# Kernel optimization log

Measured on AMD Instinct MI355X. Metric: run time of the kernel, lower is better.

Reference implementation:

```python
import jax, jax.numpy as jnp
import numpy as np

H, N, D_IN, DK, DG = 16, 128, 256, 128, 64  # heads, boxes, appearance dim, key dim, geo dim

def setup_inputs() -> dict:
    key = jax.random.key(0)
    ks = jax.random.split(key, 6)
    return {
        "f_a": jax.random.normal(ks[0], (N, D_IN), dtype=jnp.float32),
        "position_embedding": jax.random.uniform(ks[1], (N, N, DG), dtype=jnp.float32),
        "WG": jax.random.normal(ks[2], (H, DG), dtype=jnp.float32) * 0.1,
        "bg": jnp.zeros((H,), dtype=jnp.float32),
        "WK": jax.random.normal(ks[3], (H, D_IN, DK), dtype=jnp.float32) * 0.05,
        "bk": jnp.zeros((H, DK), dtype=jnp.float32),
        "WQ": jax.random.normal(ks[4], (H, D_IN, DK), dtype=jnp.float32) * 0.05,
        "bq": jnp.zeros((H, DK), dtype=jnp.float32),
        "WV": jax.random.normal(ks[5], (H, D_IN, DK), dtype=jnp.float32) * 0.05,
        "bv": jnp.zeros((H, DK), dtype=jnp.float32),
    }

def reference(f_a, position_embedding, WG, bg, WK, bk, WQ, bq, WV, bv):
    # geometric gate: relu(pos @ WG + bg), per head -> (H, N, N)
    w_g = jax.nn.relu(jnp.einsum("mng,hg->hmn", position_embedding, WG) + bg[:, None, None])
    # projections for all heads at once: (H, N, DK)
    k = jnp.einsum("nd,hdk->hnk", f_a, WK) + bk[:, None, :]
    q = jnp.einsum("nd,hdk->hnk", f_a, WQ) + bq[:, None, :]
    v = jnp.einsum("nd,hdk->hnk", f_a, WV) + bv[:, None, :]
    # score[h,m,n] = k_m . q_n / sqrt(DK)   (note: keys index rows, queries index cols)
    score = jnp.einsum("hmk,hnk->hmn", k, q) / np.sqrt(DK).astype(np.float32)
    # log-clamped geometric bias, softmax over dim=1 of the (N,N) map == last axis here
    w_mn = jax.nn.softmax(jnp.log(jnp.clip(w_g, 1e-6, None)) + score, axis=-1)
    # original broadcast (N,N)*(N,1,DK) with N==DK then sum over -2 reduces to a column sum:
    # out[h,i,k] = v[h,i,k] * sum_j w_mn[h,j,k]
    colsum = jnp.sum(w_mn, axis=1)              # (H, DK)
    out = v * colsum[:, None, :]                 # (H, N, DK)
    concat = jnp.transpose(out, (1, 0, 2)).reshape(N, H * DK)  # (N, H*DK)
    # concat.view(N, H*DK, 1) + f_a (N, D_IN) broadcasts to (N, H*DK, D_IN)
    return concat[:, :, None] + f_a[:, None, :]
```

## Files before the change

### kernel.cpp

```cpp
#include <hip/hip_runtime.h>
#include <hip/hip_bf16.h>

#define H_   16
#define N_   128
#define DIN  256
#define DK_  128
#define DG_  64
#define HNK  (H_ * N_ * DK_)

using bf16 = __hip_bfloat16;

__device__ __forceinline__ float bf2f(unsigned short u) {
    union { unsigned int i; float f; } c;
    c.i = ((unsigned int)u) << 16;
    return c.f;
}
__device__ __forceinline__ unsigned short f2bf(float f) {
    union { float f; unsigned int i; } c;
    c.f = f;
    unsigned int r = c.i + 0x7fffu + ((c.i >> 16) & 1u);
    return (unsigned short)(r >> 16);
}

template<int BF>
__device__ __forceinline__ float lde(const void* p, int i) {
    if (BF) return bf2f(((const unsigned short*)p)[i]);
    else    return ((const float*)p)[i];
}

__global__ __launch_bounds__(64) void detect_init_kernel(
    const unsigned int* __restrict__ pos, int* __restrict__ flag,
    float* __restrict__ colsum)
{
    int t = threadIdx.x;
    int cnt = 0;
#pragma unroll
    for (int i = 0; i < 4; ++i) {
        unsigned int w = pos[t * 4 + i];
        cnt += ((w & 0xffffu) <= 0x3F80u) ? 1 : 0;
    }
#pragma unroll
    for (int off = 32; off > 0; off >>= 1) cnt += __shfl_xor(cnt, off, 64);
    if (t == 0) flag[0] = (cnt >= 192) ? 1 : 0;

    float4 z = make_float4(0.f, 0.f, 0.f, 0.f);
    float4* cs = (float4*)colsum;
#pragma unroll
    for (int i = 0; i < 8; ++i) cs[t + 64 * i] = z;
}

template<int BF>
__device__ __forceinline__ void proj_body(
    const void* __restrict__ fa, const void* __restrict__ W,
    const void* __restrict__ b, float* __restrict__ out, int h, int m0)
{
    int c = threadIdx.x;
    __shared__ float fa_s[4][DIN];
    for (int i = threadIdx.x; i < 4 * DIN; i += 128) {
        int r = i >> 8, d = i & 255;
        fa_s[r][d] = lde<BF>(fa, (m0 + r) * DIN + d);
    }
    __syncthreads();

    int wbase = h * DIN * DK_ + c;
    float a0 = 0.f, a1 = 0.f, a2 = 0.f, a3 = 0.f;
    for (int d = 0; d < DIN; ++d) {
        float w = lde<BF>(W, wbase + d * DK_);
        a0 += fa_s[0][d] * w;
        a1 += fa_s[1][d] * w;
        a2 += fa_s[2][d] * w;
        a3 += fa_s[3][d] * w;
    }
    float bb = lde<BF>(b, h * DK_ + c);
    float* o = out + (h * N_ + m0) * DK_ + c;
    o[0 * DK_] = a0 + bb;
    o[1 * DK_] = a1 + bb;
    o[2 * DK_] = a2 + bb;
    o[3 * DK_] = a3 + bb;
}

__global__ __launch_bounds__(128) void proj_kernel(
    const void* __restrict__ fa,
    const void* __restrict__ WK, const void* __restrict__ bk,
    const void* __restrict__ WQ, const void* __restrict__ bq,
    const void* __restrict__ WV, const void* __restrict__ bv,
    float* __restrict__ ws, const int* __restrict__ flag)
{
    int bx = blockIdx.x;
    int which = bx / (H_ * 32);
    int rem = bx - which * (H_ * 32);
    int h = rem >> 5;
    int m0 = (rem & 31) * 4;

    const void* W; const void* b; float* out;
    if (which == 0)      { W = WK; b = bk; out = ws; }
    else if (which == 1) { W = WQ; b = bq; out = ws + HNK; }
    else                 { W = WV; b = bv; out = ws + 2 * HNK; }

    if (flag[0]) proj_body<1>(fa, W, b, out, h, m0);
    else         proj_body<0>(fa, W, b, out, h, m0);
}

template<int BF>
__device__ __forceinline__ void score_body(
    const void* __restrict__ pos, const void* __restrict__ WG,
    const void* __restrict__ bg, const float* __restrict__ ws,
    float* __restrict__ colsum, int h, int m)
{
    int n = threadIdx.x;
    __shared__ float wg_s[DG_];
    __shared__ float krow[DK_];
    __shared__ float redmax[2];
    __shared__ float redsum[2];

    if (n < DG_) wg_s[n] = lde<BF>(WG, h * DG_ + n);
    krow[n] = ws[(h * N_ + m) * DK_ + n];
    __syncthreads();

    float g = lde<BF>(bg, h);
    if (BF) {
        const uint4* pv = (const uint4*)((const unsigned short*)pos + (m * N_ + n) * DG_);
#pragma unroll
        for (int i = 0; i < 8; ++i) {
            uint4 u = pv[i];
            unsigned int uu[4] = { u.x, u.y, u.z, u.w };
#pragma unroll
            for (int j = 0; j < 4; ++j) {
                g += bf2f((unsigned short)(uu[j] & 0xffffu)) * wg_s[i * 8 + j * 2];
                g += bf2f((unsigned short)(uu[j] >> 16))     * wg_s[i * 8 + j * 2 + 1];
            }
        }
    } else {
        const float4* pv = (const float4*)((const float*)pos + (m * N_ + n) * DG_);
#pragma unroll
        for (int i = 0; i < 16; ++i) {
            float4 u = pv[i];
            g += u.x * wg_s[4 * i] + u.y * wg_s[4 * i + 1]
               + u.z * wg_s[4 * i + 2] + u.w * wg_s[4 * i + 3];
        }
    }
    float lg = logf(fmaxf(fmaxf(g, 0.0f), 1e-6f));

    const float4* qv = (const float4*)(ws + HNK + (h * N_ + n) * DK_);
    float s = 0.f;
#pragma unroll 8
    for (int i = 0; i < 32; ++i) {
        float4 q4 = qv[i];
        s += q4.x * krow[4 * i] + q4.y * krow[4 * i + 1]
           + q4.z * krow[4 * i + 2] + q4.w * krow[4 * i + 3];
    }
    float z = lg + s * 0.08838834764831845f;

    float v = z;
#pragma unroll
    for (int off = 32; off > 0; off >>= 1) v = fmaxf(v, __shfl_xor(v, off, 64));
    int wave = n >> 6;
    if ((n & 63) == 0) redmax[wave] = v;
    __syncthreads();
    float M = fmaxf(redmax[0], redmax[1]);
    float e = expf(z - M);
    float t = e;
#pragma unroll
    for (int off = 32; off > 0; off >>= 1) t += __shfl_xor(t, off, 64);
    if ((n & 63) == 0) redsum[wave] = t;
    __syncthreads();
    float S = redsum[0] + redsum[1];
    float w = e / S;

    atomicAdd(&colsum[h * DK_ + n], w);
}

__global__ __launch_bounds__(128) void score_kernel(
    const void* __restrict__ pos,
    const void* __restrict__ WG, const void* __restrict__ bg,
    const float* __restrict__ ws, float* __restrict__ colsum,
    const int* __restrict__ flag)
{
    int h = blockIdx.x >> 7;
    int m = blockIdx.x & 127;
    if (flag[0]) score_body<1>(pos, WG, bg, ws, colsum, h, m);
    else         score_body<0>(pos, WG, bg, ws, colsum, h, m);
}

__global__ __launch_bounds__(256) void out_kernel(
    const void* __restrict__ fa, const float* __restrict__ ws,
    const float* __restrict__ colsum, void* __restrict__ out,
    const int* __restrict__ flag)
{
    int e = (blockIdx.x * 256 + threadIdx.x) * 8;
    int d0  = e & 255;
    int col = (e >> 8) & 2047;
    int n   = e >> 19;
    int h = col >> 7;
    int c = col & 127;

    const float* V = ws + 2 * HNK;
    float a = V[(h * N_ + n) * DK_ + c] * colsum[h * DK_ + c];

    if (flag[0]) {
        uint4 u = *(const uint4*)((const unsigned short*)fa + n * DIN + d0);
        unsigned int uu[4] = { u.x, u.y, u.z, u.w };
        unsigned int rr[4];
#pragma unroll
        for (int j = 0; j < 4; ++j) {
            float lo = bf2f((unsigned short)(uu[j] & 0xffffu)) + a;
            float hi = bf2f((unsigned short)(uu[j] >> 16)) + a;
            rr[j] = (unsigned int)f2bf(lo) | ((unsigned int)f2bf(hi) << 16);
        }
        *(uint4*)((unsigned short*)out + e) = make_uint4(rr[0], rr[1], rr[2], rr[3]);
    } else {
        const float4* fv = (const float4*)((const float*)fa + n * DIN + d0);
        float4 u0 = fv[0], u1 = fv[1];
        u0.x += a; u0.y += a; u0.z += a; u0.w += a;
        u1.x += a; u1.y += a; u1.z += a; u1.w += a;
        float4* ov = (float4*)((float*)out + e);
        ov[0] = u0;
        ov[1] = u1;
    }
}

extern "C" void kernel_launch(void* const* d_in, const int* in_sizes, int n_in,
                              void* d_out, int out_size, void* d_ws, size_t ws_size,
                              hipStream_t stream)
{
    const void* fa  = d_in[0];
    const void* pos = d_in[1];
    const void* WG  = d_in[2];
    const void* bg  = d_in[3];
    const void* WK  = d_in[4];
    const void* bk  = d_in[5];
    const void* WQ  = d_in[6];
    const void* bq  = d_in[7];
    const void* WV  = d_in[8];
    const void* bv  = d_in[9];

    int*   flag = (int*)d_ws;
    float* buf  = (float*)d_ws + 16;
    float* colsum = buf + 3 * HNK;

    hipLaunchKernelGGL(detect_init_kernel, dim3(1), dim3(64), 0, stream,
                       (const unsigned int*)pos, flag, colsum);

    hipLaunchKernelGGL(proj_kernel, dim3(3 * H_ * 32), dim3(128), 0, stream,
                       fa, WK, bk, WQ, bq, WV, bv, buf, flag);

    hipLaunchKernelGGL(score_kernel, dim3(H_ * N_), dim3(128), 0, stream,
                       pos, WG, bg, buf, colsum, flag);

    const int nblk = (N_ * H_ * DK_ * DIN) / (8 * 256);
    hipLaunchKernelGGL(out_kernel, dim3(nblk), dim3(256), 0, stream,
                       fa, buf, colsum, d_out, flag);
}
```

Baseline: 339.3 us.

## Drop detect/init kernel, inline dtype detection, vectorize LDS reads, nontemporal output stores

Removes the separate detect_init launch: each kernel now detects bf16 from the first 32 words of pos itself, and colsum zeroing moves into the first blocks of proj_kernel. LDS reads in the projection and score loops become 4-wide vector loads, logf/expf are replaced by the fast intrinsics, and the large output writes use nontemporal stores. The aim is to cut one launch plus serialization and to reduce memory and instruction overhead in the bandwidth-bound output kernel. Each thread now repeats a 32-word detection read, and the fast math intrinsics are less precise.

```diff
diff --git a/kernel.cpp b/kernel.cpp
--- a/kernel.cpp
+++ b/kernel.cpp
@@ -1,5 +1,4 @@
 #include <hip/hip_runtime.h>
-#include <hip/hip_bf16.h>
 
 #define H_   16
 #define N_   128
@@ -8,7 +7,8 @@
 #define DG_  64
 #define HNK  (H_ * N_ * DK_)
 
-using bf16 = __hip_bfloat16;
+typedef float        f32x4 __attribute__((ext_vector_type(4)));
+typedef unsigned int u32x4 __attribute__((ext_vector_type(4)));
 
 __device__ __forceinline__ float bf2f(unsigned short u) {
     union { unsigned int i; float f; } c;
@@ -28,25 +28,13 @@
     else    return ((const float*)p)[i];
 }
 
-__global__ __launch_bounds__(64) void detect_init_kernel(
-    const unsigned int* __restrict__ pos, int* __restrict__ flag,
-    float* __restrict__ colsum)
-{
-    int t = threadIdx.x;
+__device__ __forceinline__ int detect_bf16(const void* __restrict__ pos) {
+    const unsigned int* p = (const unsigned int*)pos;
     int cnt = 0;
 #pragma unroll
-    for (int i = 0; i < 4; ++i) {
-        unsigned int w = pos[t * 4 + i];
-        cnt += ((w & 0xffffu) <= 0x3F80u) ? 1 : 0;
-    }
-#pragma unroll
-    for (int off = 32; off > 0; off >>= 1) cnt += __shfl_xor(cnt, off, 64);
-    if (t == 0) flag[0] = (cnt >= 192) ? 1 : 0;
-
-    float4 z = make_float4(0.f, 0.f, 0.f, 0.f);
-    float4* cs = (float4*)colsum;
-#pragma unroll
-    for (int i = 0; i < 8; ++i) cs[t + 64 * i] = z;
+    for (int i = 0; i < 32; ++i)
+        cnt += ((p[i] & 0xffffu) <= 0x3F80u) ? 1 : 0;
+    return cnt >= 24;
 }
 
 template<int BF>
@@ -55,7 +43,7 @@
     const void* __restrict__ b, float* __restrict__ out, int h, int m0)
 {
     int c = threadIdx.x;
-    __shared__ float fa_s[4][DIN];
+    __shared__ __align__(16) float fa_s[4][DIN];
     for (int i = threadIdx.x; i < 4 * DIN; i += 128) {
         int r = i >> 8, d = i & 255;
         fa_s[r][d] = lde<BF>(fa, (m0 + r) * DIN + d);
@@ -64,12 +52,22 @@
 
     int wbase = h * DIN * DK_ + c;
     float a0 = 0.f, a1 = 0.f, a2 = 0.f, a3 = 0.f;
-    for (int d = 0; d < DIN; ++d) {
-        float w = lde<BF>(W, wbase + d * DK_);
-        a0 += fa_s[0][d] * w;
-        a1 += fa_s[1][d] * w;
-        a2 += fa_s[2][d] * w;
-        a3 += fa_s[3][d] * w;
+    const f32x4* f0 = (const f32x4*)fa_s[0];
+    const f32x4* f1 = (const f32x4*)fa_s[1];
+    const f32x4* f2 = (const f32x4*)fa_s[2];
+    const f32x4* f3 = (const f32x4*)fa_s[3];
+#pragma unroll 4
+    for (int dq = 0; dq < DIN / 4; ++dq) {
+        int d = dq * 4;
+        float w0 = lde<BF>(W, wbase + (d + 0) * DK_);
+        float w1 = lde<BF>(W, wbase + (d + 1) * DK_);
+        float w2 = lde<BF>(W, wbase + (d + 2) * DK_);
+        float w3 = lde<BF>(W, wbase + (d + 3) * DK_);
+        f32x4 x0 = f0[dq], x1 = f1[dq], x2 = f2[dq], x3 = f3[dq];
+        a0 += w0 * x0[0] + w1 * x0[1] + w2 * x0[2] + w3 * x0[3];
+        a1 += w0 * x1[0] + w1 * x1[1] + w2 * x1[2] + w3 * x1[3];
+        a2 += w0 * x2[0] + w1 * x2[1] + w2 * x2[2] + w3 * x2[3];
+        a3 += w0 * x3[0] + w1 * x3[1] + w2 * x3[2] + w3 * x3[3];
     }
     float bb = lde<BF>(b, h * DK_ + c);
     float* o = out + (h * N_ + m0) * DK_ + c;
@@ -80,13 +78,15 @@
 }
 
 __global__ __launch_bounds__(128) void proj_kernel(
-    const void* __restrict__ fa,
+    const void* __restrict__ fa, const void* __restrict__ pos,
     const void* __restrict__ WK, const void* __restrict__ bk,
     const void* __restrict__ WQ, const void* __restrict__ bq,
     const void* __restrict__ WV, const void* __restrict__ bv,
-    float* __restrict__ ws, const int* __restrict__ flag)
+    float* __restrict__ ws, float* __restrict__ colsum)
 {
     int bx = blockIdx.x;
+    if (bx < 16) colsum[bx * 128 + threadIdx.x] = 0.f;
+
     int which = bx / (H_ * 32);
     int rem = bx - which * (H_ * 32);
     int h = rem >> 5;
@@ -97,8 +97,8 @@
     else if (which == 1) { W = WQ; b = bq; out = ws + HNK; }
     else                 { W = WV; b = bv; out = ws + 2 * HNK; }
 
-    if (flag[0]) proj_body<1>(fa, W, b, out, h, m0);
-    else         proj_body<0>(fa, W, b, out, h, m0);
+    if (detect_bf16(pos)) proj_body<1>(fa, W, b, out, h, m0);
+    else                  proj_body<0>(fa, W, b, out, h, m0);
 }
 
 template<int BF>
@@ -108,8 +108,8 @@
     float* __restrict__ colsum, int h, int m)
 {
     int n = threadIdx.x;
-    __shared__ float wg_s[DG_];
-    __shared__ float krow[DK_];
+    __shared__ __align__(16) float wg_s[DG_];
+    __shared__ __align__(16) float krow[DK_];
     __shared__ float redmax[2];
     __shared__ float redsum[2];
 
@@ -132,22 +132,24 @@
         }
     } else {
         const float4* pv = (const float4*)((const float*)pos + (m * N_ + n) * DG_);
+        const f32x4* wv = (const f32x4*)wg_s;
 #pragma unroll
         for (int i = 0; i < 16; ++i) {
             float4 u = pv[i];
-            g += u.x * wg_s[4 * i] + u.y * wg_s[4 * i + 1]
-               + u.z * wg_s[4 * i + 2] + u.w * wg_s[4 * i + 3];
+            f32x4 wq = wv[i];
+            g += u.x * wq[0] + u.y * wq[1] + u.z * wq[2] + u.w * wq[3];
         }
     }
-    float lg = logf(fmaxf(fmaxf(g, 0.0f), 1e-6f));
+    float lg = __logf(fmaxf(fmaxf(g, 0.0f), 1e-6f));
 
     const float4* qv = (const float4*)(ws + HNK + (h * N_ + n) * DK_);
+    const f32x4* kv = (const f32x4*)krow;
     float s = 0.f;
 #pragma unroll 8
     for (int i = 0; i < 32; ++i) {
         float4 q4 = qv[i];
-        s += q4.x * krow[4 * i] + q4.y * krow[4 * i + 1]
-           + q4.z * krow[4 * i + 2] + q4.w * krow[4 * i + 3];
+        f32x4 k4 = kv[i];
+        s += q4.x * k4[0] + q4.y * k4[1] + q4.z * k4[2] + q4.w * k4[3];
     }
     float z = lg + s * 0.08838834764831845f;
 
@@ -158,7 +160,7 @@
     if ((n & 63) == 0) redmax[wave] = v;
     __syncthreads();
     float M = fmaxf(redmax[0], redmax[1]);
-    float e = expf(z - M);
+    float e = __expf(z - M);
     float t = e;
 #pragma unroll
     for (int off = 32; off > 0; off >>= 1) t += __shfl_xor(t, off, 64);
@@ -173,19 +175,18 @@
 __global__ __launch_bounds__(128) void score_kernel(
     const void* __restrict__ pos,
     const void* __restrict__ WG, const void* __restrict__ bg,
-    const float* __restrict__ ws, float* __restrict__ colsum,
-    const int* __restrict__ flag)
+    const float* __restrict__ ws, float* __restrict__ colsum)
 {
     int h = blockIdx.x >> 7;
     int m = blockIdx.x & 127;
-    if (flag[0]) score_body<1>(pos, WG, bg, ws, colsum, h, m);
-    else         score_body<0>(pos, WG, bg, ws, colsum, h, m);
+    if (detect_bf16(pos)) score_body<1>(pos, WG, bg, ws, colsum, h, m);
+    else                  score_body<0>(pos, WG, bg, ws, colsum, h, m);
 }
 
 __global__ __launch_bounds__(256) void out_kernel(
-    const void* __restrict__ fa, const float* __restrict__ ws,
-    const float* __restrict__ colsum, void* __restrict__ out,
-    const int* __restrict__ flag)
+    const void* __restrict__ fa, const void* __restrict__ pos,
+    const float* __restrict__ ws, const float* __restrict__ colsum,
+    void* __restrict__ out)
 {
     int e = (blockIdx.x * 256 + threadIdx.x) * 8;
     int d0  = e & 255;
@@ -197,25 +198,24 @@
     const float* V = ws + 2 * HNK;
     float a = V[(h * N_ + n) * DK_ + c] * colsum[h * DK_ + c];
 
-    if (flag[0]) {
-        uint4 u = *(const uint4*)((const unsigned short*)fa + n * DIN + d0);
-        unsigned int uu[4] = { u.x, u.y, u.z, u.w };
-        unsigned int rr[4];
+    if (detect_bf16(pos)) {
+        u32x4 u = *(const u32x4*)((const unsigned short*)fa + n * DIN + d0);
+        u32x4 rr;
 #pragma unroll
         for (int j = 0; j < 4; ++j) {
-            float lo = bf2f((unsigned short)(uu[j] & 0xffffu)) + a;
-            float hi = bf2f((unsigned short)(uu[j] >> 16)) + a;
+            float lo = bf2f((unsigned short)(u[j] & 0xffffu)) + a;
+            float hi = bf2f((unsigned short)(u[j] >> 16)) + a;
             rr[j] = (unsigned int)f2bf(lo) | ((unsigned int)f2bf(hi) << 16);
         }
-        *(uint4*)((unsigned short*)out + e) = make_uint4(rr[0], rr[1], rr[2], rr[3]);
+        __builtin_nontemporal_store(rr, (u32x4*)((unsigned short*)out + e));
     } else {
-        const float4* fv = (const float4*)((const float*)fa + n * DIN + d0);
-        float4 u0 = fv[0], u1 = fv[1];
-        u0.x += a; u0.y += a; u0.z += a; u0.w += a;
-        u1.x += a; u1.y += a; u1.z += a; u1.w += a;
-        float4* ov = (float4*)((float*)out + e);
-        ov[0] = u0;
-        ov[1] = u1;
+        const f32x4* fv = (const f32x4*)((const float*)fa + n * DIN + d0);
+        f32x4 u0 = fv[0], u1 = fv[1];
+        u0 += a;
+        u1 += a;
+        f32x4* ov = (f32x4*)((float*)out + e);
+        __builtin_nontemporal_store(u0, ov);
+        __builtin_nontemporal_store(u1, ov + 1);
     }
 }
 
@@ -234,20 +234,16 @@
     const void* WV  = d_in[8];
     const void* bv  = d_in[9];
 
-    int*   flag = (int*)d_ws;
-    float* buf  = (float*)d_ws + 16;
+    float* buf    = (float*)d_ws;
     float* colsum = buf + 3 * HNK;
 
-    hipLaunchKernelGGL(detect_init_kernel, dim3(1), dim3(64), 0, stream,
-                       (const unsigned int*)pos, flag, colsum);
-
     hipLaunchKernelGGL(proj_kernel, dim3(3 * H_ * 32), dim3(128), 0, stream,
-                       fa, WK, bk, WQ, bq, WV, bv, buf, flag);
+                       fa, pos, WK, bk, WQ, bq, WV, bv, buf, colsum);
 
     hipLaunchKernelGGL(score_kernel, dim3(H_ * N_), dim3(128), 0, stream,
-                       pos, WG, bg, buf, colsum, flag);
+                       pos, WG, bg, buf, colsum);
 
     const int nblk = (N_ * H_ * DK_ * DIN) / (8 * 256);
     hipLaunchKernelGGL(out_kernel, dim3(nblk), dim3(256), 0, stream,
-                       fa, buf, colsum, d_out, flag);
-}
+                       fa, pos, buf, colsum, d_out);
+}
```

After: 393.3 us. 15.9% more time.
